# Kernel tuning notes

Measured on AMD Instinct MI355X. Metric: run time of the kernel, lower is better.

Reference implementation:

```python
import jax, jax.numpy as jnp
import numpy as np

N, M, Z_DIM = 32768, 8192, 64


def setup_inputs() -> dict:
    key = jax.random.key(0)
    kz, ke = jax.random.split(key)
    z = jax.random.normal(kz, (N, Z_DIM), dtype=jnp.float32)
    # torch: e = rand(M, z_dim) * 2 - 1  -> uniform in [-1, 1)
    e = jax.random.uniform(ke, (M, Z_DIM), dtype=jnp.float32, minval=-1.0, maxval=1.0)
    return {"z": z, "e": e}


def reference(z, e):
    # data['z'] = tanh(z)
    zt = jnp.tanh(z)                                   # (N, Z)
    # pairwise squared distance via Gram expansion:
    # ||a - b||^2 = ||a||^2 + ||b||^2 - 2 a.b  (same math as the
    # broadcasted sum((a-b)**2) without the (N, M, Z) intermediate)
    zn = jnp.sum(zt * zt, axis=1)                      # (N,)
    en = jnp.sum(e * e, axis=1)                        # (M,)
    distance = zn[:, None] + en[None, :] - 2.0 * (zt @ e.T)   # (N, M)
    # min over the batch dim N for each sample e, then mean over M
    loss = jnp.mean(jnp.min(distance, axis=0))
    return loss
```

## Files before the change

### kernel.cpp

```cpp
#include <hip/hip_runtime.h>
#include <hip/hip_bf16.h>
#include <math.h>

#define NN 32768
#define MM 8192
#define ZD 64
#define WAVES 4
#define MW 64
#define MBLK (WAVES * MW)
#define NMB (MM / MBLK)
#define NCHUNKS 32
#define CHUNK (NN / NCHUNKS)
#define NROWS 64
#define NITER (CHUNK / NROWS)

typedef __attribute__((ext_vector_type(8))) short bf16x8;
typedef __attribute__((ext_vector_type(4))) float f32x4;

__device__ inline unsigned short f2bf(float f) {
  unsigned u = __float_as_uint(f);
  return (unsigned short)((u + 0x7fffu + ((u >> 16) & 1u)) >> 16);
}
__device__ inline float bf2f(unsigned short h) {
  return __uint_as_float(((unsigned)h) << 16);
}

__global__ __launch_bounds__(256) void prep_z(const float* __restrict__ z,
                                              unsigned short* __restrict__ zb,
                                              float* __restrict__ zn) {
  const int row = blockIdx.x * 32 + (threadIdx.x >> 3);
  const int q = threadIdx.x & 7;
  const size_t base = (size_t)row * ZD + q * 8;
  float4 v0 = *reinterpret_cast<const float4*>(&z[base]);
  float4 v1 = *reinterpret_cast<const float4*>(&z[base + 4]);
  float in[8] = {v0.x, v0.y, v0.z, v0.w, v1.x, v1.y, v1.z, v1.w};
  unsigned short b[8];
  float s = 0.f;
#pragma unroll
  for (int i = 0; i < 8; ++i) {
    b[i] = f2bf(tanhf(in[i]));
    float r = bf2f(b[i]);
    s += r * r;
  }
  *reinterpret_cast<bf16x8*>(&zb[base]) = *reinterpret_cast<bf16x8*>(b);
  s += __shfl_xor(s, 1, 64);
  s += __shfl_xor(s, 2, 64);
  s += __shfl_xor(s, 4, 64);
  if (q == 0) zn[row] = s;
}

__global__ __launch_bounds__(256) void prep_e(const float* __restrict__ e,
                                              unsigned short* __restrict__ eb,
                                              float* __restrict__ en) {
  const int row = blockIdx.x * 32 + (threadIdx.x >> 3);
  const int q = threadIdx.x & 7;
  const size_t base = (size_t)row * ZD + q * 8;
  float4 v0 = *reinterpret_cast<const float4*>(&e[base]);
  float4 v1 = *reinterpret_cast<const float4*>(&e[base + 4]);
  float in[8] = {v0.x, v0.y, v0.z, v0.w, v1.x, v1.y, v1.z, v1.w};
  unsigned short b[8];
  float s = 0.f;
#pragma unroll
  for (int i = 0; i < 8; ++i) {
    unsigned short qb = f2bf(in[i]);
    float r = bf2f(qb);
    s += r * r;
    b[i] = f2bf(-2.f * r);
  }
  *reinterpret_cast<bf16x8*>(&eb[base]) = *reinterpret_cast<bf16x8*>(b);
  s += __shfl_xor(s, 1, 64);
  s += __shfl_xor(s, 2, 64);
  s += __shfl_xor(s, 4, 64);
  if (q == 0) en[row] = s;
}

__global__ __launch_bounds__(256, 4) void min_dist(
    const unsigned short* __restrict__ zb, const unsigned short* __restrict__ eb,
    const float* __restrict__ zn, float* __restrict__ partial) {
  __shared__ __align__(128) unsigned short zlds[2][NROWS * ZD];
  const int wg = ((blockIdx.x & 7) << 7) + (blockIdx.x >> 3);
  const int mb = wg & (NMB - 1);
  const int cb = wg >> 5;
  const int lane = threadIdx.x & 63;
  const int wv = threadIdx.x >> 6;
  const int lr = lane & 15;
  const int lg = lane >> 4;
  const int m0 = mb * MBLK + wv * MW;
  const int nb0 = cb * CHUNK;

  const int srow = lane >> 3;
  const int sslot = (lane & 7) ^ srow;
  const char* zsrc = (const char*)zb + (size_t)nb0 * 128 +
                     (wv * 16 + srow) * 128 + (sslot << 4);
  char* ldst0 = (char*)&zlds[0][0] + wv * 2048;
  char* ldst1 = (char*)&zlds[1][0] + wv * 2048;

  bf16x8 bfr[4][2];
#pragma unroll
  for (int t = 0; t < 4; ++t)
#pragma unroll
    for (int h = 0; h < 2; ++h)
      bfr[t][h] = *reinterpret_cast<const bf16x8*>(
          &eb[(size_t)(m0 + t * 16 + lr) * ZD + h * 32 + lg * 8]);

  f32x4 minv[4];
#pragma unroll
  for (int t = 0; t < 4; ++t)
    minv[t] = (f32x4){3.4e38f, 3.4e38f, 3.4e38f, 3.4e38f};

  auto stage = [&](char* dst, const char* src) {
    __builtin_amdgcn_global_load_lds(
        (const __attribute__((address_space(1))) unsigned int*)src,
        (__attribute__((address_space(3))) unsigned int*)dst, 16, 0, 0);
    __builtin_amdgcn_global_load_lds(
        (const __attribute__((address_space(1))) unsigned int*)(src + 1024),
        (__attribute__((address_space(3))) unsigned int*)(dst + 1024), 16, 0, 0);
  };

  const float* znp = zn + nb0;
  const int x0 = (lg * 16) ^ ((lr & 7) << 4);

  stage(ldst0, zsrc);
  zsrc += 8192;
  __syncthreads();

  for (int it = 0; it < NITER; ++it) {
    const char* lbase = (it & 1) ? (const char*)&zlds[1][0] : (const char*)&zlds[0][0];
    if (it + 1 < NITER) {
      stage((it & 1) ? ldst0 : ldst1, zsrc);
      zsrc += 8192;
    }
#pragma unroll
    for (int s = 0; s < 4; ++s) {
      const int rb = (s * 16 + lr) * 128;
      bf16x8 a0 = *reinterpret_cast<const bf16x8*>(lbase + rb + x0);
      bf16x8 a1 = *reinterpret_cast<const bf16x8*>(lbase + rb + (x0 ^ 64));
      f32x4 znv = *reinterpret_cast<const f32x4*>(znp + s * 16 + lg * 4);
#pragma unroll
      for (int t = 0; t < 4; ++t) {
        f32x4 acc = __builtin_amdgcn_mfma_f32_16x16x32_bf16(a0, bfr[t][0], znv, 0, 0, 0);
        acc = __builtin_amdgcn_mfma_f32_16x16x32_bf16(a1, bfr[t][1], acc, 0, 0, 0);
#pragma unroll
        for (int r = 0; r < 4; ++r) minv[t][r] = fminf(minv[t][r], acc[r]);
      }
    }
    znp += NROWS;
    __syncthreads();
  }

#pragma unroll
  for (int t = 0; t < 4; ++t) {
    float v = fminf(fminf(minv[t][0], minv[t][1]), fminf(minv[t][2], minv[t][3]));
    v = fminf(v, __shfl_xor(v, 16, 64));
    v = fminf(v, __shfl_xor(v, 32, 64));
    if (lg == 0) partial[(size_t)cb * MM + m0 + t * 16 + lr] = v;
  }
}

__global__ __launch_bounds__(256) void finalize1(const float* __restrict__ partial,
                                                 const float* __restrict__ en,
                                                 double* __restrict__ bsum) {
  const int m = blockIdx.x * 256 + threadIdx.x;
  float mv = partial[m];
#pragma unroll
  for (int c = 1; c < NCHUNKS; ++c)
    mv = fminf(mv, partial[(size_t)c * MM + m]);
  double s = (double)(mv + en[m]);
  __shared__ double sred[256];
  sred[threadIdx.x] = s;
  __syncthreads();
  for (int off = 128; off > 0; off >>= 1) {
    if ((int)threadIdx.x < off) sred[threadIdx.x] += sred[threadIdx.x + off];
    __syncthreads();
  }
  if (threadIdx.x == 0) bsum[blockIdx.x] = sred[0];
}

__global__ __launch_bounds__(64) void finalize2(const double* __restrict__ bsum,
                                                float* __restrict__ out) {
  double s = (threadIdx.x < MM / 256) ? bsum[threadIdx.x] : 0.0;
  s += __shfl_xor(s, 1, 64);
  s += __shfl_xor(s, 2, 64);
  s += __shfl_xor(s, 4, 64);
  s += __shfl_xor(s, 8, 64);
  s += __shfl_xor(s, 16, 64);
  s += __shfl_xor(s, 32, 64);
  if (threadIdx.x == 0) out[0] = (float)(s / (double)MM);
}

extern "C" void kernel_launch(void* const* d_in, const int* in_sizes, int n_in,
                              void* d_out, int out_size, void* d_ws, size_t ws_size,
                              hipStream_t stream) {
  const float* z = (const float*)d_in[0];
  const float* e = (const float*)d_in[1];
  float* out = (float*)d_out;

  unsigned short* zb = (unsigned short*)d_ws;
  unsigned short* eb = zb + (size_t)NN * ZD;
  float* zn = (float*)(eb + (size_t)MM * ZD);
  float* en = zn + NN;
  float* partial = en + MM;
  double* bsum = (double*)(partial + (size_t)NCHUNKS * MM);

  prep_z<<<NN / 32, 256, 0, stream>>>(z, zb, zn);
  prep_e<<<MM / 32, 256, 0, stream>>>(e, eb, en);
  min_dist<<<NMB * NCHUNKS, 256, 0, stream>>>(zb, eb, zn, partial);
  finalize1<<<MM / 256, 256, 0, stream>>>(partial, en, bsum);
  finalize2<<<1, 64, 0, stream>>>(bsum, out);
}
```

Before: 49.22 us.

## Merge prep kernels, double LDS tile rows, collapse per-tile min to scalar

Merges the two preprocessing kernels into one launch that dispatches on block index, removing one kernel launch. Doubles the number of z rows staged per LDS iteration to 128, halving the count of loop iterations and barriers while doubling LDS use per block. Reduces the per-tile running minimum from a 4-wide vector to a scalar, cutting registers and min instructions. The larger LDS footprint may lower occupancy.

```diff
diff --git a/kernel.cpp b/kernel.cpp
--- a/kernel.cpp
+++ b/kernel.cpp
@@ -11,7 +11,7 @@
 #define NMB (MM / MBLK)
 #define NCHUNKS 32
 #define CHUNK (NN / NCHUNKS)
-#define NROWS 64
+#define NROWS 128
 #define NITER (CHUNK / NROWS)
 
 typedef __attribute__((ext_vector_type(8))) short bf16x8;
@@ -25,53 +25,51 @@
   return __uint_as_float(((unsigned)h) << 16);
 }
 
-__global__ __launch_bounds__(256) void prep_z(const float* __restrict__ z,
-                                              unsigned short* __restrict__ zb,
-                                              float* __restrict__ zn) {
-  const int row = blockIdx.x * 32 + (threadIdx.x >> 3);
+__global__ __launch_bounds__(256) void prep(
+    const float* __restrict__ z, const float* __restrict__ e,
+    unsigned short* __restrict__ zb, float* __restrict__ zn,
+    unsigned short* __restrict__ eb, float* __restrict__ en) {
   const int q = threadIdx.x & 7;
-  const size_t base = (size_t)row * ZD + q * 8;
-  float4 v0 = *reinterpret_cast<const float4*>(&z[base]);
-  float4 v1 = *reinterpret_cast<const float4*>(&z[base + 4]);
-  float in[8] = {v0.x, v0.y, v0.z, v0.w, v1.x, v1.y, v1.z, v1.w};
-  unsigned short b[8];
-  float s = 0.f;
-#pragma unroll
-  for (int i = 0; i < 8; ++i) {
-    b[i] = f2bf(tanhf(in[i]));
-    float r = bf2f(b[i]);
-    s += r * r;
-  }
-  *reinterpret_cast<bf16x8*>(&zb[base]) = *reinterpret_cast<bf16x8*>(b);
-  s += __shfl_xor(s, 1, 64);
-  s += __shfl_xor(s, 2, 64);
-  s += __shfl_xor(s, 4, 64);
-  if (q == 0) zn[row] = s;
-}
-
-__global__ __launch_bounds__(256) void prep_e(const float* __restrict__ e,
-                                              unsigned short* __restrict__ eb,
-                                              float* __restrict__ en) {
-  const int row = blockIdx.x * 32 + (threadIdx.x >> 3);
-  const int q = threadIdx.x & 7;
-  const size_t base = (size_t)row * ZD + q * 8;
-  float4 v0 = *reinterpret_cast<const float4*>(&e[base]);
-  float4 v1 = *reinterpret_cast<const float4*>(&e[base + 4]);
-  float in[8] = {v0.x, v0.y, v0.z, v0.w, v1.x, v1.y, v1.z, v1.w};
-  unsigned short b[8];
-  float s = 0.f;
-#pragma unroll
-  for (int i = 0; i < 8; ++i) {
-    unsigned short qb = f2bf(in[i]);
-    float r = bf2f(qb);
-    s += r * r;
-    b[i] = f2bf(-2.f * r);
-  }
-  *reinterpret_cast<bf16x8*>(&eb[base]) = *reinterpret_cast<bf16x8*>(b);
-  s += __shfl_xor(s, 1, 64);
-  s += __shfl_xor(s, 2, 64);
-  s += __shfl_xor(s, 4, 64);
-  if (q == 0) en[row] = s;
+  if (blockIdx.x < NN / 32) {
+    const int row = blockIdx.x * 32 + (threadIdx.x >> 3);
+    const size_t base = (size_t)row * ZD + q * 8;
+    float4 v0 = *reinterpret_cast<const float4*>(&z[base]);
+    float4 v1 = *reinterpret_cast<const float4*>(&z[base + 4]);
+    float in[8] = {v0.x, v0.y, v0.z, v0.w, v1.x, v1.y, v1.z, v1.w};
+    unsigned short b[8];
+    float s = 0.f;
+#pragma unroll
+    for (int i = 0; i < 8; ++i) {
+      b[i] = f2bf(tanhf(in[i]));
+      float r = bf2f(b[i]);
+      s += r * r;
+    }
+    *reinterpret_cast<bf16x8*>(&zb[base]) = *reinterpret_cast<bf16x8*>(b);
+    s += __shfl_xor(s, 1, 64);
+    s += __shfl_xor(s, 2, 64);
+    s += __shfl_xor(s, 4, 64);
+    if (q == 0) zn[row] = s;
+  } else {
+    const int row = (blockIdx.x - NN / 32) * 32 + (threadIdx.x >> 3);
+    const size_t base = (size_t)row * ZD + q * 8;
+    float4 v0 = *reinterpret_cast<const float4*>(&e[base]);
+    float4 v1 = *reinterpret_cast<const float4*>(&e[base + 4]);
+    float in[8] = {v0.x, v0.y, v0.z, v0.w, v1.x, v1.y, v1.z, v1.w};
+    unsigned short b[8];
+    float s = 0.f;
+#pragma unroll
+    for (int i = 0; i < 8; ++i) {
+      unsigned short qb = f2bf(in[i]);
+      float r = bf2f(qb);
+      s += r * r;
+      b[i] = f2bf(-2.f * r);
+    }
+    *reinterpret_cast<bf16x8*>(&eb[base]) = *reinterpret_cast<bf16x8*>(b);
+    s += __shfl_xor(s, 1, 64);
+    s += __shfl_xor(s, 2, 64);
+    s += __shfl_xor(s, 4, 64);
+    if (q == 0) en[row] = s;
+  }
 }
 
 __global__ __launch_bounds__(256, 4) void min_dist(
@@ -91,9 +89,9 @@
   const int srow = lane >> 3;
   const int sslot = (lane & 7) ^ srow;
   const char* zsrc = (const char*)zb + (size_t)nb0 * 128 +
-                     (wv * 16 + srow) * 128 + (sslot << 4);
-  char* ldst0 = (char*)&zlds[0][0] + wv * 2048;
-  char* ldst1 = (char*)&zlds[1][0] + wv * 2048;
+                     (wv * 32 + srow) * 128 + (sslot << 4);
+  char* ldst0 = (char*)&zlds[0][0] + wv * 4096;
+  char* ldst1 = (char*)&zlds[1][0] + wv * 4096;
 
   bf16x8 bfr[4][2];
 #pragma unroll
@@ -103,35 +101,32 @@
       bfr[t][h] = *reinterpret_cast<const bf16x8*>(
           &eb[(size_t)(m0 + t * 16 + lr) * ZD + h * 32 + lg * 8]);
 
-  f32x4 minv[4];
-#pragma unroll
-  for (int t = 0; t < 4; ++t)
-    minv[t] = (f32x4){3.4e38f, 3.4e38f, 3.4e38f, 3.4e38f};
+  float minv[4] = {3.4e38f, 3.4e38f, 3.4e38f, 3.4e38f};
 
   auto stage = [&](char* dst, const char* src) {
-    __builtin_amdgcn_global_load_lds(
-        (const __attribute__((address_space(1))) unsigned int*)src,
-        (__attribute__((address_space(3))) unsigned int*)dst, 16, 0, 0);
-    __builtin_amdgcn_global_load_lds(
-        (const __attribute__((address_space(1))) unsigned int*)(src + 1024),
-        (__attribute__((address_space(3))) unsigned int*)(dst + 1024), 16, 0, 0);
+#pragma unroll
+    for (int j = 0; j < 4; ++j)
+      __builtin_amdgcn_global_load_lds(
+          (const __attribute__((address_space(1))) unsigned int*)(src + j * 1024),
+          (__attribute__((address_space(3))) unsigned int*)(dst + j * 1024),
+          16, 0, 0);
   };
 
   const float* znp = zn + nb0;
   const int x0 = (lg * 16) ^ ((lr & 7) << 4);
 
   stage(ldst0, zsrc);
-  zsrc += 8192;
+  zsrc += NROWS * 128;
   __syncthreads();
 
   for (int it = 0; it < NITER; ++it) {
     const char* lbase = (it & 1) ? (const char*)&zlds[1][0] : (const char*)&zlds[0][0];
     if (it + 1 < NITER) {
       stage((it & 1) ? ldst0 : ldst1, zsrc);
-      zsrc += 8192;
-    }
-#pragma unroll
-    for (int s = 0; s < 4; ++s) {
+      zsrc += NROWS * 128;
+    }
+#pragma unroll
+    for (int s = 0; s < NROWS / 16; ++s) {
       const int rb = (s * 16 + lr) * 128;
       bf16x8 a0 = *reinterpret_cast<const bf16x8*>(lbase + rb + x0);
       bf16x8 a1 = *reinterpret_cast<const bf16x8*>(lbase + rb + (x0 ^ 64));
@@ -140,8 +135,8 @@
       for (int t = 0; t < 4; ++t) {
         f32x4 acc = __builtin_amdgcn_mfma_f32_16x16x32_bf16(a0, bfr[t][0], znv, 0, 0, 0);
         acc = __builtin_amdgcn_mfma_f32_16x16x32_bf16(a1, bfr[t][1], acc, 0, 0, 0);
-#pragma unroll
-        for (int r = 0; r < 4; ++r) minv[t][r] = fminf(minv[t][r], acc[r]);
+        float x = fminf(fminf(acc[0], acc[1]), acc[2]);
+        minv[t] = fminf(fminf(x, acc[3]), minv[t]);
       }
     }
     znp += NROWS;
@@ -150,7 +145,7 @@
 
 #pragma unroll
   for (int t = 0; t < 4; ++t) {
-    float v = fminf(fminf(minv[t][0], minv[t][1]), fminf(minv[t][2], minv[t][3]));
+    float v = minv[t];
     v = fminf(v, __shfl_xor(v, 16, 64));
     v = fminf(v, __shfl_xor(v, 32, 64));
     if (lg == 0) partial[(size_t)cb * MM + m0 + t * 16 + lr] = v;
@@ -202,8 +197,7 @@
   float* partial = en + MM;
   double* bsum = (double*)(partial + (size_t)NCHUNKS * MM);
 
-  prep_z<<<NN / 32, 256, 0, stream>>>(z, zb, zn);
-  prep_e<<<MM / 32, 256, 0, stream>>>(e, eb, en);
+  prep<<<(NN + MM) / 32, 256, 0, stream>>>(z, e, zb, zn, eb, en);
   min_dist<<<NMB * NCHUNKS, 256, 0, stream>>>(zb, eb, zn, partial);
   finalize1<<<MM / 256, 256, 0, stream>>>(partial, en, bsum);
   finalize2<<<1, 64, 0, stream>>>(bsum, out);
```

Result: faster. 46.90 us (-4.7%).
